# Performance work log

Hardware: AMD Instinct MI355X
Metric: run time of the kernel (lower is better)

Reference implementation:

```python
import jax, jax.numpy as jnp
import numpy as np

DIM = 256
HEADS = 8
SR = 2
EPS = 1e-5


def setup_inputs() -> dict:
    key = jax.random.key(0)
    ks = jax.random.split(key, 8)
    B, N, C = 4, 4096, DIM
    s = 0.02
    return {
        "x": jax.random.normal(ks[0], (B, N, C), dtype=jnp.float32),
        "H": 64,
        "W": 64,
        # sequence-reduction conv (Conv2d dim->dim, k=SR, stride=SR), OIHW
        "sr_w": jax.random.normal(ks[1], (C, C, SR, SR), dtype=jnp.float32) * s,
        "sr_b": jnp.zeros((C,), dtype=jnp.float32),
        "ln_g": jnp.ones((C,), dtype=jnp.float32),
        "ln_b": jnp.zeros((C,), dtype=jnp.float32),
        # torch Linear weights: y = x @ W.T (qkv_bias=False)
        "q_w": jax.random.normal(ks[2], (C, C), dtype=jnp.float32) * s,
        "kv_w": jax.random.normal(ks[3], (2 * C, C), dtype=jnp.float32) * s,
        "proj_w": jax.random.normal(ks[4], (C, C), dtype=jnp.float32) * s,
        "proj_b": jnp.zeros((C,), dtype=jnp.float32),
    }


def reference(x, H, W, sr_w, sr_b, ln_g, ln_b, q_w, kv_w, proj_w, proj_b):
    B, N, C = x.shape
    h, d = HEADS, C // HEADS
    scale = d ** -0.5

    # q: [B, h, N, d]
    q = (x @ q_w.T).reshape(B, N, h, d).transpose(0, 2, 1, 3)

    # sequence reduction: [B,N,C] -> [B,C,H,W] -> conv(k=SR, s=SR) -> [B, N', C]
    x_ = x.transpose(0, 2, 1).reshape(B, C, H, W)
    x_ = jax.lax.conv_general_dilated(
        x_, sr_w, window_strides=(SR, SR), padding="VALID",
        dimension_numbers=("NCHW", "OIHW", "NCHW"))
    x_ = x_ + sr_b[None, :, None, None]
    x_ = x_.reshape(B, C, -1).transpose(0, 2, 1)  # [B, N', C]

    # LayerNorm over C
    mu = x_.mean(-1, keepdims=True)
    var = x_.var(-1, keepdims=True)
    x_ = (x_ - mu) * jax.lax.rsqrt(var + EPS) * ln_g + ln_b

    # kv: [2, B, h, N', d]
    kv = (x_ @ kv_w.T).reshape(B, -1, 2, h, d).transpose(2, 0, 3, 1, 4)
    k, v = kv[0], kv[1]

    attn = jnp.einsum("bhnd,bhmd->bhnm", q, k) * scale
    attn = jax.nn.softmax(attn, axis=-1)  # attn_drop = 0 -> identity
    out = jnp.einsum("bhnm,bhmd->bhnd", attn, v)
    out = out.transpose(0, 2, 1, 3).reshape(B, N, C)

    return out @ proj_w.T + proj_b  # proj_drop = 0 -> identity
```

## Files before the change

### kernel.cpp

```cpp
#include <hip/hip_runtime.h>
#include <hip/hip_bf16.h>


typedef __attribute__((ext_vector_type(8))) short bf16x8;
typedef __attribute__((ext_vector_type(8))) unsigned short u16x8;
typedef __attribute__((ext_vector_type(4))) float f32x4;
typedef __attribute__((ext_vector_type(16))) float f32x16;
typedef __attribute__((ext_vector_type(2))) unsigned u32x2v;
typedef __attribute__((ext_vector_type(4))) unsigned u32x4v;

__device__ inline unsigned short f2bf(float f) {
  unsigned u = __float_as_uint(f);
  u += 0x7fffu + ((u >> 16) & 1u);
  return (unsigned short)(u >> 16);
}

__global__ __launch_bounds__(256) void prep_kernel(
    const float* __restrict__ srw, unsigned short* __restrict__ srw_bf) {
  const int o = blockIdx.x, t = threadIdx.x;
  float4 v = reinterpret_cast<const float4*>(srw + (size_t)o * 1024)[t];
  srw_bf[(size_t)o * 1024 + 0 * 256 + t] = f2bf(v.x);
  srw_bf[(size_t)o * 1024 + 1 * 256 + t] = f2bf(v.y);
  srw_bf[(size_t)o * 1024 + 2 * 256 + t] = f2bf(v.z);
  srw_bf[(size_t)o * 1024 + 3 * 256 + t] = f2bf(v.w);
}

__device__ __forceinline__ void gemm_body_q(
    const float* __restrict__ Af, const float* __restrict__ W,
    unsigned short* __restrict__ C, int K, int N, float oscale,
    int m0, int n0, unsigned short* Asb, unsigned short* Bsb) {
  const int tid = threadIdx.x;
  const int w = tid >> 6, l = tid & 63, c = l & 15, g = l >> 4;
  const int wr = w >> 1, wc = w & 1;
  const int ar = tid >> 1, ah = tid & 1;
  const int bn = tid >> 2, bq = tid & 3;

  f32x4 acc[4][2];
#pragma unroll
  for (int mt = 0; mt < 4; ++mt)
#pragma unroll
    for (int nt = 0; nt < 2; ++nt)
#pragma unroll
      for (int r = 0; r < 4; ++r) acc[mt][nt][r] = 0.f;

  for (int k0 = 0; k0 < K; k0 += 32) {
    __syncthreads();
    {
      const float* asrc = Af + (size_t)(m0 + ar) * K + k0 + ah * 16;
      float4 a0 = *reinterpret_cast<const float4*>(asrc);
      float4 a1 = *reinterpret_cast<const float4*>(asrc + 4);
      float4 a2 = *reinterpret_cast<const float4*>(asrc + 8);
      float4 a3 = *reinterpret_cast<const float4*>(asrc + 12);
      u16x8 w0, w1;
      w0[0] = f2bf(a0.x); w0[1] = f2bf(a0.y); w0[2] = f2bf(a0.z); w0[3] = f2bf(a0.w);
      w0[4] = f2bf(a1.x); w0[5] = f2bf(a1.y); w0[6] = f2bf(a1.z); w0[7] = f2bf(a1.w);
      w1[0] = f2bf(a2.x); w1[1] = f2bf(a2.y); w1[2] = f2bf(a2.z); w1[3] = f2bf(a2.w);
      w1[4] = f2bf(a3.x); w1[5] = f2bf(a3.y); w1[6] = f2bf(a3.z); w1[7] = f2bf(a3.w);
      *reinterpret_cast<u16x8*>(&Asb[ar * 40 + ah * 16]) = w0;
      *reinterpret_cast<u16x8*>(&Asb[ar * 40 + ah * 16 + 8]) = w1;
    }
    {
      const float* wsrc = W + (size_t)(n0 + bn) * K + k0 + bq * 8;
      float4 w0 = *reinterpret_cast<const float4*>(wsrc);
      float4 w1 = *reinterpret_cast<const float4*>(wsrc + 4);
      u16x8 wb;
      wb[0] = f2bf(w0.x); wb[1] = f2bf(w0.y); wb[2] = f2bf(w0.z); wb[3] = f2bf(w0.w);
      wb[4] = f2bf(w1.x); wb[5] = f2bf(w1.y); wb[6] = f2bf(w1.z); wb[7] = f2bf(w1.w);
      *reinterpret_cast<u16x8*>(&Bsb[bn * 40 + bq * 8]) = wb;
    }
    __syncthreads();
    bf16x8 af[4], bfr[2];
#pragma unroll
    for (int mt = 0; mt < 4; ++mt)
      af[mt] = *reinterpret_cast<const bf16x8*>(
          &Asb[(wr * 64 + mt * 16 + c) * 40 + g * 8]);
#pragma unroll
    for (int nt = 0; nt < 2; ++nt)
      bfr[nt] = *reinterpret_cast<const bf16x8*>(
          &Bsb[(wc * 32 + nt * 16 + c) * 40 + g * 8]);
#pragma unroll
    for (int mt = 0; mt < 4; ++mt)
#pragma unroll
      for (int nt = 0; nt < 2; ++nt)
        acc[mt][nt] = __builtin_amdgcn_mfma_f32_16x16x32_bf16(
            af[mt], bfr[nt], acc[mt][nt], 0, 0, 0);
  }

#pragma unroll
  for (int mt = 0; mt < 4; ++mt)
#pragma unroll
    for (int nt = 0; nt < 2; ++nt) {
      int row = m0 + wr * 64 + mt * 16 + g * 4;
      int col = n0 + wc * 32 + nt * 16 + c;
#pragma unroll
      for (int r = 0; r < 4; ++r)
        C[(size_t)(row + r) * N + col] = f2bf(acc[mt][nt][r] * oscale);
    }
}

__device__ __forceinline__ void conv_body(
    const float* __restrict__ Xf, const unsigned short* __restrict__ Wp,
    const float* __restrict__ bias, float* __restrict__ C,
    int m0, int n0, unsigned short* Asb, unsigned short* Bsb) {
  const int tid = threadIdx.x;
  const int w = tid >> 6, l = tid & 63, c = l & 15, g = l >> 4;
  const int wr = w >> 1, wc = w & 1;
  const int sr = tid >> 2, sh = tid & 3;

  int base[4];
  {
    int row = m0 + sr;
    int b = row >> 10, o = row & 1023, oh = o >> 5, ow = o & 31;
#pragma unroll
    for (int tap = 0; tap < 4; ++tap) {
      int n = ((oh << 1) + (tap >> 1)) * 64 + (ow << 1) + (tap & 1);
      base[tap] = ((b << 12) + n) << 8;
    }
  }

  f32x4 acc[2][2];
#pragma unroll
  for (int mt = 0; mt < 2; ++mt)
#pragma unroll
    for (int nt = 0; nt < 2; ++nt)
#pragma unroll
      for (int r = 0; r < 4; ++r) acc[mt][nt][r] = 0.f;

  for (int k0 = 0; k0 < 1024; k0 += 32) {
    const int tap = k0 >> 8, ci0 = (k0 & 255) + sh * 8;
    __syncthreads();
    {
      const float* xp = Xf + base[tap] + ci0;
      float4 a0 = *reinterpret_cast<const float4*>(xp);
      float4 a1 = *reinterpret_cast<const float4*>(xp + 4);
      u16x8 av;
      av[0] = f2bf(a0.x); av[1] = f2bf(a0.y); av[2] = f2bf(a0.z); av[3] = f2bf(a0.w);
      av[4] = f2bf(a1.x); av[5] = f2bf(a1.y); av[6] = f2bf(a1.z); av[7] = f2bf(a1.w);
      *reinterpret_cast<u16x8*>(&Asb[sr * 40 + sh * 8]) = av;
    }
    u16x8 wv = *reinterpret_cast<const u16x8*>(
        &Wp[(size_t)(n0 + sr) * 1024 + k0 + sh * 8]);
    *reinterpret_cast<u16x8*>(&Bsb[sr * 40 + sh * 8]) = wv;
    __syncthreads();
    bf16x8 af[2], bfr[2];
#pragma unroll
    for (int mt = 0; mt < 2; ++mt)
      af[mt] = *reinterpret_cast<const bf16x8*>(
          &Asb[(wr * 32 + mt * 16 + c) * 40 + g * 8]);
#pragma unroll
    for (int nt = 0; nt < 2; ++nt)
      bfr[nt] = *reinterpret_cast<const bf16x8*>(
          &Bsb[(wc * 32 + nt * 16 + c) * 40 + g * 8]);
#pragma unroll
    for (int mt = 0; mt < 2; ++mt)
#pragma unroll
      for (int nt = 0; nt < 2; ++nt)
        acc[mt][nt] = __builtin_amdgcn_mfma_f32_16x16x32_bf16(
            af[mt], bfr[nt], acc[mt][nt], 0, 0, 0);
  }

#pragma unroll
  for (int mt = 0; mt < 2; ++mt)
#pragma unroll
    for (int nt = 0; nt < 2; ++nt) {
      int row = m0 + wr * 32 + mt * 16 + g * 4;
      int col = n0 + wc * 32 + nt * 16 + c;
      float bv = bias[col];
#pragma unroll
      for (int r = 0; r < 4; ++r)
        C[(size_t)(row + r) * 256 + col] = acc[mt][nt][r] + bv;
    }
}

__global__ __launch_bounds__(256) void qconv_kernel(
    const float* __restrict__ x, const float* __restrict__ q_w,
    unsigned short* __restrict__ q_bf, const unsigned short* __restrict__ srw_bf,
    const float* __restrict__ sr_b, float* __restrict__ xred, float qscale) {
  __shared__ unsigned short smem[128 * 40 + 64 * 40];
  const int bid = blockIdx.x;
  if (bid < 512) {
    gemm_body_q(x, q_w, q_bf, 256, 256, qscale,
                (bid >> 2) * 128, (bid & 3) * 64, smem, smem + 128 * 40);
  } else {
    int cb = bid - 512;
    conv_body(x, srw_bf, sr_b, xred,
              (cb >> 2) * 64, (cb & 3) * 64, smem, smem + 64 * 40);
  }
}

__global__ __launch_bounds__(256) void kv_gemm(
    const unsigned short* __restrict__ A, const float* __restrict__ W,
    unsigned short* __restrict__ Kb, unsigned short* __restrict__ Vtp) {
  __shared__ unsigned short Asb[128 * 40];
  __shared__ unsigned short Bsb[64 * 40];
  const int tid = threadIdx.x;
  const int w = tid >> 6, l = tid & 63, c = l & 15, g = l >> 4;
  const int wr = w >> 1, wc = w & 1;
  const int m0 = blockIdx.y * 128, n0 = blockIdx.x * 64;
  const int ar = tid >> 1, ah = tid & 1;
  const int bn = tid >> 2, bq = tid & 3;
  const int K = 256;

  f32x4 acc[4][2];
#pragma unroll
  for (int mt = 0; mt < 4; ++mt)
#pragma unroll
    for (int nt = 0; nt < 2; ++nt)
#pragma unroll
      for (int r = 0; r < 4; ++r) acc[mt][nt][r] = 0.f;

  for (int k0 = 0; k0 < K; k0 += 32) {
    __syncthreads();
    {
      const unsigned short* asrc = A + (size_t)(m0 + ar) * K + k0 + ah * 16;
      u16x8 a0 = *reinterpret_cast<const u16x8*>(asrc);
      u16x8 a1 = *reinterpret_cast<const u16x8*>(asrc + 8);
      *reinterpret_cast<u16x8*>(&Asb[ar * 40 + ah * 16]) = a0;
      *reinterpret_cast<u16x8*>(&Asb[ar * 40 + ah * 16 + 8]) = a1;
    }
    {
      const float* wsrc = W + (size_t)(n0 + bn) * K + k0 + bq * 8;
      float4 w0 = *reinterpret_cast<const float4*>(wsrc);
      float4 w1 = *reinterpret_cast<const float4*>(wsrc + 4);
      u16x8 wb;
      wb[0] = f2bf(w0.x); wb[1] = f2bf(w0.y); wb[2] = f2bf(w0.z); wb[3] = f2bf(w0.w);
      wb[4] = f2bf(w1.x); wb[5] = f2bf(w1.y); wb[6] = f2bf(w1.z); wb[7] = f2bf(w1.w);
      *reinterpret_cast<u16x8*>(&Bsb[bn * 40 + bq * 8]) = wb;
    }
    __syncthreads();
    bf16x8 af[4], bfr[2];
#pragma unroll
    for (int mt = 0; mt < 4; ++mt)
      af[mt] = *reinterpret_cast<const bf16x8*>(
          &Asb[(wr * 64 + mt * 16 + c) * 40 + g * 8]);
#pragma unroll
    for (int nt = 0; nt < 2; ++nt)
      bfr[nt] = *reinterpret_cast<const bf16x8*>(
          &Bsb[(wc * 32 + nt * 16 + c) * 40 + g * 8]);
#pragma unroll
    for (int mt = 0; mt < 4; ++mt)
#pragma unroll
      for (int nt = 0; nt < 2; ++nt)
        acc[mt][nt] = __builtin_amdgcn_mfma_f32_16x16x32_bf16(
            af[mt], bfr[nt], acc[mt][nt], 0, 0, 0);
  }

#pragma unroll
  for (int mt = 0; mt < 4; ++mt)
#pragma unroll
    for (int nt = 0; nt < 2; ++nt) {
      int row = m0 + wr * 64 + mt * 16 + g * 4;
      int col = n0 + wc * 32 + nt * 16 + c;
#pragma unroll
      for (int r = 0; r < 4; ++r) {
        float v = acc[mt][nt][r];
        if (col < 256) {
          Kb[(size_t)(row + r) * 256 + col] = f2bf(v);
        } else {
          int head = (col - 256) >> 5, d = (col - 256) & 31;
          int rr = row + r;
          Vtp[((size_t)(((rr >> 10) << 3) + head) * 32 + d) * 1024 +
              (rr & 1023)] = f2bf(v);
        }
      }
    }
}

__global__ __launch_bounds__(256) void proj_gemm(
    const unsigned short* __restrict__ A, const float* __restrict__ W,
    const float* __restrict__ bias, float* __restrict__ C) {
  __shared__ unsigned short Asb[64 * 40];
  __shared__ unsigned short Bsb[64 * 40];
  const int tid = threadIdx.x;
  const int w = tid >> 6, l = tid & 63, c = l & 15, g = l >> 4;
  const int wr = w >> 1, wc = w & 1;
  const int m0 = blockIdx.y * 64, n0 = blockIdx.x * 64;
  const int sr = tid >> 2, sh = tid & 3;

  f32x4 acc[2][2];
#pragma unroll
  for (int mt = 0; mt < 2; ++mt)
#pragma unroll
    for (int nt = 0; nt < 2; ++nt)
#pragma unroll
      for (int r = 0; r < 4; ++r) acc[mt][nt][r] = 0.f;

  for (int k0 = 0; k0 < 256; k0 += 32) {
    __syncthreads();
    {
      u16x8 av = *reinterpret_cast<const u16x8*>(
          &A[(size_t)(m0 + sr) * 256 + k0 + sh * 8]);
      *reinterpret_cast<u16x8*>(&Asb[sr * 40 + sh * 8]) = av;
    }
    {
      const float* wsrc = W + (size_t)(n0 + sr) * 256 + k0 + sh * 8;
      float4 w0 = *reinterpret_cast<const float4*>(wsrc);
      float4 w1 = *reinterpret_cast<const float4*>(wsrc + 4);
      u16x8 wb;
      wb[0] = f2bf(w0.x); wb[1] = f2bf(w0.y); wb[2] = f2bf(w0.z); wb[3] = f2bf(w0.w);
      wb[4] = f2bf(w1.x); wb[5] = f2bf(w1.y); wb[6] = f2bf(w1.z); wb[7] = f2bf(w1.w);
      *reinterpret_cast<u16x8*>(&Bsb[sr * 40 + sh * 8]) = wb;
    }
    __syncthreads();
    bf16x8 af[2], bfr[2];
#pragma unroll
    for (int mt = 0; mt < 2; ++mt)
      af[mt] = *reinterpret_cast<const bf16x8*>(
          &Asb[(wr * 32 + mt * 16 + c) * 40 + g * 8]);
#pragma unroll
    for (int nt = 0; nt < 2; ++nt)
      bfr[nt] = *reinterpret_cast<const bf16x8*>(
          &Bsb[(wc * 32 + nt * 16 + c) * 40 + g * 8]);
#pragma unroll
    for (int mt = 0; mt < 2; ++mt)
#pragma unroll
      for (int nt = 0; nt < 2; ++nt)
        acc[mt][nt] = __builtin_amdgcn_mfma_f32_16x16x32_bf16(
            af[mt], bfr[nt], acc[mt][nt], 0, 0, 0);
  }

#pragma unroll
  for (int mt = 0; mt < 2; ++mt)
#pragma unroll
    for (int nt = 0; nt < 2; ++nt) {
      int row = m0 + wr * 32 + mt * 16 + g * 4;
      int col = n0 + wc * 32 + nt * 16 + c;
      float bv = bias[col];
#pragma unroll
      for (int r = 0; r < 4; ++r)
        C[(size_t)(row + r) * 256 + col] = acc[mt][nt][r] + bv;
    }
}

__global__ __launch_bounds__(256) void ln_kernel(
    const float* __restrict__ xr, const float* __restrict__ gam,
    const float* __restrict__ bet, unsigned short* __restrict__ xo) {
  const int w = threadIdx.x >> 6, l = threadIdx.x & 63;
  const int row = blockIdx.x * 4 + w;
  float4 v = *reinterpret_cast<const float4*>(xr + (size_t)row * 256 + l * 4);
  float s = (v.x + v.y) + (v.z + v.w);
  float s2 = (v.x * v.x + v.y * v.y) + (v.z * v.z + v.w * v.w);
#pragma unroll
  for (int off = 32; off > 0; off >>= 1) {
    s  += __shfl_xor(s, off, 64);
    s2 += __shfl_xor(s2, off, 64);
  }
  float mean = s * (1.f / 256.f);
  float var = s2 * (1.f / 256.f) - mean * mean;
  float rstd = rsqrtf(var + 1e-5f);
  float4 g = *reinterpret_cast<const float4*>(gam + l * 4);
  float4 bb = *reinterpret_cast<const float4*>(bet + l * 4);
  unsigned short o0 = f2bf((v.x - mean) * rstd * g.x + bb.x);
  unsigned short o1 = f2bf((v.y - mean) * rstd * g.y + bb.y);
  unsigned short o2 = f2bf((v.z - mean) * rstd * g.z + bb.z);
  unsigned short o3 = f2bf((v.w - mean) * rstd * g.w + bb.w);
  unsigned long long pk =
      (unsigned long long)o0 | ((unsigned long long)o1 << 16) |
      ((unsigned long long)o2 << 32) | ((unsigned long long)o3 << 48);
  *reinterpret_cast<unsigned long long*>(xo + (size_t)row * 256 + l * 4) = pk;
}

__global__ __launch_bounds__(256) void attn_mfma(
    const unsigned short* __restrict__ Qb,
    const unsigned short* __restrict__ Kb,
    const unsigned short* __restrict__ Vtg,
    unsigned short* __restrict__ O) {
  __shared__ __align__(16) unsigned short Kt[2][64][36];
  __shared__ __align__(16) unsigned short Vt[2][32][72];

  const int tid = threadIdx.x;
  const int l = tid & 63;
  const int w = tid >> 6;
  const int q32 = l & 31, hi = l >> 5;
  const int wg = blockIdx.x;
  const int qb = wg & 31, head = (wg >> 5) & 7, b = wg >> 8;
  const int hcol = head << 5;
  const int q0 = (b << 12) + (qb << 7) + (w << 5);

  bf16x8 qf[2];
  {
    const unsigned short* qp = Qb + (size_t)(q0 + q32) * 256 + hcol + hi * 8;
    qf[0] = *reinterpret_cast<const bf16x8*>(qp);
    qf[1] = *reinterpret_cast<const bf16x8*>(qp + 16);
  }

  const int sd = tid >> 3, skv = (tid & 7) << 3;
  const unsigned short* vtrow =
      Vtg + ((size_t)((b << 3) + head) * 32 + sd) * 1024 + skv;
  const int kr = tid >> 2, kh = (tid & 3) << 3;
  const unsigned short* ktrow =
      Kb + ((size_t)(b << 10) + kr) * 256 + hcol + kh;

  {
    u16x8 va = *reinterpret_cast<const u16x8*>(vtrow);
    *reinterpret_cast<u16x8*>(&Vt[0][sd][skv]) = va;
    u16x8 ka = *reinterpret_cast<const u16x8*>(ktrow);
    *reinterpret_cast<u16x8*>(&Kt[0][kr][kh]) = ka;
  }

  f32x16 acc;
#pragma unroll
  for (int r = 0; r < 16; ++r) acc[r] = 0.f;
  float lsum = 0.f;

  for (int t = 0; t < 16; ++t) {
    const int cur = t & 1;
    __syncthreads();

    u16x8 nv0, nk0;
    if (t < 15) {
      nv0 = *reinterpret_cast<const u16x8*>(vtrow + (t + 1) * 64);
      nk0 = *reinterpret_cast<const u16x8*>(ktrow + (size_t)(t + 1) * 64 * 256);
    }

    f32x16 s[2];
    {
      bf16x8 k00 = *reinterpret_cast<const bf16x8*>(&Kt[cur][q32][hi * 8]);
      bf16x8 k01 = *reinterpret_cast<const bf16x8*>(&Kt[cur][q32][hi * 8 + 16]);
      bf16x8 k10 = *reinterpret_cast<const bf16x8*>(&Kt[cur][q32 + 32][hi * 8]);
      bf16x8 k11 = *reinterpret_cast<const bf16x8*>(&Kt[cur][q32 + 32][hi * 8 + 16]);
      f32x16 z;
#pragma unroll
      for (int r = 0; r < 16; ++r) z[r] = 0.f;
      s[0] = __builtin_amdgcn_mfma_f32_32x32x16_bf16(k00, qf[0], z, 0, 0, 0);
      s[0] = __builtin_amdgcn_mfma_f32_32x32x16_bf16(k01, qf[1], s[0], 0, 0, 0);
      s[1] = __builtin_amdgcn_mfma_f32_32x32x16_bf16(k10, qf[0], z, 0, 0, 0);
      s[1] = __builtin_amdgcn_mfma_f32_32x32x16_bf16(k11, qf[1], s[1], 0, 0, 0);
    }

#pragma unroll
    for (int kvb = 0; kvb < 2; ++kvb) {
      float p16[16];
#pragma unroll
      for (int r = 0; r < 16; ++r)
        p16[r] = __builtin_amdgcn_exp2f(s[kvb][r]);
      float s0 = (p16[0] + p16[1]) + (p16[2] + p16[3]);
      float s1 = (p16[4] + p16[5]) + (p16[6] + p16[7]);
      float s2 = (p16[8] + p16[9]) + (p16[10] + p16[11]);
      float s3 = (p16[12] + p16[13]) + (p16[14] + p16[15]);
      lsum += (s0 + s1) + (s2 + s3);
      unsigned A[8];
#pragma unroll
      for (int i = 0; i < 8; ++i) {
        unsigned o;
        asm("v_cvt_pk_bf16_f32 %0, %1, %2"
            : "=v"(o) : "v"(p16[2 * i]), "v"(p16[2 * i + 1]));
        A[i] = o;
      }
      u32x2v r02 = __builtin_amdgcn_permlane32_swap(A[0], A[2], false, false);
      u32x2v r13 = __builtin_amdgcn_permlane32_swap(A[1], A[3], false, false);
      u32x2v r46 = __builtin_amdgcn_permlane32_swap(A[4], A[6], false, false);
      u32x2v r57 = __builtin_amdgcn_permlane32_swap(A[5], A[7], false, false);
      u32x4v pk0 = {r02[0], r13[0], r02[1], r13[1]};
      u32x4v pk1 = {r46[0], r57[0], r46[1], r57[1]};
      bf16x8 pf0 = __builtin_bit_cast(bf16x8, pk0);
      bf16x8 pf1 = __builtin_bit_cast(bf16x8, pk1);
      const unsigned short* vrow = &Vt[cur][q32][kvb * 32 + hi * 8];
      bf16x8 vf0 = *reinterpret_cast<const bf16x8*>(vrow);
      bf16x8 vf1 = *reinterpret_cast<const bf16x8*>(vrow + 16);
      acc = __builtin_amdgcn_mfma_f32_32x32x16_bf16(vf0, pf0, acc, 0, 0, 0);
      acc = __builtin_amdgcn_mfma_f32_32x32x16_bf16(vf1, pf1, acc, 0, 0, 0);
    }

    if (t < 15) {
      *reinterpret_cast<u16x8*>(&Vt[cur ^ 1][sd][skv]) = nv0;
      *reinterpret_cast<u16x8*>(&Kt[cur ^ 1][kr][kh]) = nk0;
    }
  }

  lsum += __shfl_xor(lsum, 32, 64);
  float inv = 1.f / lsum;
  unsigned short* orow = O + (size_t)(q0 + q32) * 256 + hcol;
#pragma unroll
  for (int rb = 0; rb < 4; ++rb) {
    const int d0 = rb * 8 + hi * 4;
    float a0 = acc[rb * 4 + 0] * inv, a1 = acc[rb * 4 + 1] * inv;
    float a2 = acc[rb * 4 + 2] * inv, a3 = acc[rb * 4 + 3] * inv;
    unsigned w0, w1;
    asm("v_cvt_pk_bf16_f32 %0, %1, %2" : "=v"(w0) : "v"(a0), "v"(a1));
    asm("v_cvt_pk_bf16_f32 %0, %1, %2" : "=v"(w1) : "v"(a2), "v"(a3));
    unsigned long long pk = (unsigned long long)w0 | ((unsigned long long)w1 << 32);
    *reinterpret_cast<unsigned long long*>(orow + d0) = pk;
  }
}

extern "C" void kernel_launch(void* const* d_in, const int* in_sizes, int n_in,
                              void* d_out, int out_size, void* d_ws,
                              size_t ws_size, hipStream_t stream) {
  const float* x      = (const float*)d_in[0];
  const float* sr_w   = (const float*)d_in[3];
  const float* sr_b   = (const float*)d_in[4];
  const float* ln_g   = (const float*)d_in[5];
  const float* ln_b   = (const float*)d_in[6];
  const float* q_w    = (const float*)d_in[7];
  const float* kv_w   = (const float*)d_in[8];
  const float* proj_w = (const float*)d_in[9];
  const float* proj_b = (const float*)d_in[10];
  float* out = (float*)d_out;

  char* ws = (char*)d_ws;
  unsigned short* q_bf    = (unsigned short*)(ws);
  unsigned short* srw_bf  = (unsigned short*)(ws + 8388608);
  float*          xred    = (float*)(ws + 8912896);
  unsigned short* x_ln    = (unsigned short*)(ws + 13107200);
  unsigned short* k_buf   = (unsigned short*)(ws + 15204352);
  unsigned short* vt_buf  = (unsigned short*)(ws + 17301504);
  unsigned short* attn_bf = (unsigned short*)(ws + 19398656);

  const float qscale = 0.25506975154985854f;

  prep_kernel<<<256, 256, 0, stream>>>(sr_w, srw_bf);
  qconv_kernel<<<768, 256, 0, stream>>>(
      x, q_w, q_bf, srw_bf, sr_b, xred, qscale);
  ln_kernel<<<1024, 256, 0, stream>>>(xred, ln_g, ln_b, x_ln);
  kv_gemm<<<dim3(8, 32), 256, 0, stream>>>(x_ln, kv_w, k_buf, vt_buf);
  attn_mfma<<<1024, 256, 0, stream>>>(q_bf, k_buf, vt_buf, attn_bf);
  proj_gemm<<<dim3(4, 256), 256, 0, stream>>>(attn_bf, proj_w, proj_b, out);
}
```

Measured before the change: 92.34 us.

## Double-buffer LDS tiles with register prefetch in all GEMM and conv loops

Converts the q GEMM, conv, kv GEMM and proj GEMM main loops to double-buffered shared-memory tiles. The next K-slice is loaded from global memory into registers before the MFMAs on the current slice, then written into the alternate buffer afterwards. This leaves one barrier per iteration instead of two and hides global load latency behind the math. In exchange it doubles LDS use and raises register pressure, which may lower occupancy.

After: 88.79 us. 3.8% less time.

```diff
diff --git a/kernel.cpp b/kernel.cpp
--- a/kernel.cpp
+++ b/kernel.cpp
@@ -13,6 +13,13 @@
   unsigned u = __float_as_uint(f);
   u += 0x7fffu + ((u >> 16) & 1u);
   return (unsigned short)(u >> 16);
+}
+
+__device__ inline u16x8 cast8(float4 a, float4 b) {
+  u16x8 r;
+  r[0] = f2bf(a.x); r[1] = f2bf(a.y); r[2] = f2bf(a.z); r[3] = f2bf(a.w);
+  r[4] = f2bf(b.x); r[5] = f2bf(b.y); r[6] = f2bf(b.z); r[7] = f2bf(b.w);
+  return r;
 }
 
 __global__ __launch_bounds__(256) void prep_kernel(
@@ -27,13 +34,18 @@
 
 __device__ __forceinline__ void gemm_body_q(
     const float* __restrict__ Af, const float* __restrict__ W,
-    unsigned short* __restrict__ C, int K, int N, float oscale,
+    unsigned short* __restrict__ C, float oscale,
     int m0, int n0, unsigned short* Asb, unsigned short* Bsb) {
+  const int K = 256, N = 256, NK = 8;
   const int tid = threadIdx.x;
   const int w = tid >> 6, l = tid & 63, c = l & 15, g = l >> 4;
   const int wr = w >> 1, wc = w & 1;
   const int ar = tid >> 1, ah = tid & 1;
   const int bn = tid >> 2, bq = tid & 3;
+  const int ABUF = 128 * 40, BBUF = 64 * 40;
+
+  const float* aptr = Af + (size_t)(m0 + ar) * K + ah * 16;
+  const float* wptr = W + (size_t)(n0 + bn) * K + bq * 8;
 
   f32x4 acc[4][2];
 #pragma unroll
@@ -43,47 +55,53 @@
 #pragma unroll
       for (int r = 0; r < 4; ++r) acc[mt][nt][r] = 0.f;
 
-  for (int k0 = 0; k0 < K; k0 += 32) {
+  {
+    float4 a0 = *reinterpret_cast<const float4*>(aptr);
+    float4 a1 = *reinterpret_cast<const float4*>(aptr + 4);
+    float4 a2 = *reinterpret_cast<const float4*>(aptr + 8);
+    float4 a3 = *reinterpret_cast<const float4*>(aptr + 12);
+    float4 w0 = *reinterpret_cast<const float4*>(wptr);
+    float4 w1 = *reinterpret_cast<const float4*>(wptr + 4);
+    *reinterpret_cast<u16x8*>(&Asb[ar * 40 + ah * 16]) = cast8(a0, a1);
+    *reinterpret_cast<u16x8*>(&Asb[ar * 40 + ah * 16 + 8]) = cast8(a2, a3);
+    *reinterpret_cast<u16x8*>(&Bsb[bn * 40 + bq * 8]) = cast8(w0, w1);
+  }
+
+  for (int t = 0; t < NK; ++t) {
+    const int cur = t & 1;
     __syncthreads();
-    {
-      const float* asrc = Af + (size_t)(m0 + ar) * K + k0 + ah * 16;
-      float4 a0 = *reinterpret_cast<const float4*>(asrc);
-      float4 a1 = *reinterpret_cast<const float4*>(asrc + 4);
-      float4 a2 = *reinterpret_cast<const float4*>(asrc + 8);
-      float4 a3 = *reinterpret_cast<const float4*>(asrc + 12);
-      u16x8 w0, w1;
-      w0[0] = f2bf(a0.x); w0[1] = f2bf(a0.y); w0[2] = f2bf(a0.z); w0[3] = f2bf(a0.w);
-      w0[4] = f2bf(a1.x); w0[5] = f2bf(a1.y); w0[6] = f2bf(a1.z); w0[7] = f2bf(a1.w);
-      w1[0] = f2bf(a2.x); w1[1] = f2bf(a2.y); w1[2] = f2bf(a2.z); w1[3] = f2bf(a2.w);
-      w1[4] = f2bf(a3.x); w1[5] = f2bf(a3.y); w1[6] = f2bf(a3.z); w1[7] = f2bf(a3.w);
-      *reinterpret_cast<u16x8*>(&Asb[ar * 40 + ah * 16]) = w0;
-      *reinterpret_cast<u16x8*>(&Asb[ar * 40 + ah * 16 + 8]) = w1;
-    }
-    {
-      const float* wsrc = W + (size_t)(n0 + bn) * K + k0 + bq * 8;
-      float4 w0 = *reinterpret_cast<const float4*>(wsrc);
-      float4 w1 = *reinterpret_cast<const float4*>(wsrc + 4);
-      u16x8 wb;
-      wb[0] = f2bf(w0.x); wb[1] = f2bf(w0.y); wb[2] = f2bf(w0.z); wb[3] = f2bf(w0.w);
-      wb[4] = f2bf(w1.x); wb[5] = f2bf(w1.y); wb[6] = f2bf(w1.z); wb[7] = f2bf(w1.w);
-      *reinterpret_cast<u16x8*>(&Bsb[bn * 40 + bq * 8]) = wb;
-    }
-    __syncthreads();
+    float4 na0, na1, na2, na3, nw0, nw1;
+    if (t < NK - 1) {
+      const float* ap = aptr + (t + 1) * 32;
+      na0 = *reinterpret_cast<const float4*>(ap);
+      na1 = *reinterpret_cast<const float4*>(ap + 4);
+      na2 = *reinterpret_cast<const float4*>(ap + 8);
+      na3 = *reinterpret_cast<const float4*>(ap + 12);
+      const float* wp = wptr + (t + 1) * 32;
+      nw0 = *reinterpret_cast<const float4*>(wp);
+      nw1 = *reinterpret_cast<const float4*>(wp + 4);
+    }
     bf16x8 af[4], bfr[2];
 #pragma unroll
     for (int mt = 0; mt < 4; ++mt)
       af[mt] = *reinterpret_cast<const bf16x8*>(
-          &Asb[(wr * 64 + mt * 16 + c) * 40 + g * 8]);
+          &Asb[cur * ABUF + (wr * 64 + mt * 16 + c) * 40 + g * 8]);
 #pragma unroll
     for (int nt = 0; nt < 2; ++nt)
       bfr[nt] = *reinterpret_cast<const bf16x8*>(
-          &Bsb[(wc * 32 + nt * 16 + c) * 40 + g * 8]);
+          &Bsb[cur * BBUF + (wc * 32 + nt * 16 + c) * 40 + g * 8]);
 #pragma unroll
     for (int mt = 0; mt < 4; ++mt)
 #pragma unroll
       for (int nt = 0; nt < 2; ++nt)
         acc[mt][nt] = __builtin_amdgcn_mfma_f32_16x16x32_bf16(
             af[mt], bfr[nt], acc[mt][nt], 0, 0, 0);
+    if (t < NK - 1) {
+      const int nxt = cur ^ 1;
+      *reinterpret_cast<u16x8*>(&Asb[nxt * ABUF + ar * 40 + ah * 16]) = cast8(na0, na1);
+      *reinterpret_cast<u16x8*>(&Asb[nxt * ABUF + ar * 40 + ah * 16 + 8]) = cast8(na2, na3);
+      *reinterpret_cast<u16x8*>(&Bsb[nxt * BBUF + bn * 40 + bq * 8]) = cast8(nw0, nw1);
+    }
   }
 
 #pragma unroll
@@ -102,10 +120,12 @@
     const float* __restrict__ Xf, const unsigned short* __restrict__ Wp,
     const float* __restrict__ bias, float* __restrict__ C,
     int m0, int n0, unsigned short* Asb, unsigned short* Bsb) {
+  const int NK = 32;
   const int tid = threadIdx.x;
   const int w = tid >> 6, l = tid & 63, c = l & 15, g = l >> 4;
   const int wr = w >> 1, wc = w & 1;
   const int sr = tid >> 2, sh = tid & 3;
+  const int BUF = 64 * 40;
 
   int base[4];
   {
@@ -117,6 +137,7 @@
       base[tap] = ((b << 12) + n) << 8;
     }
   }
+  const unsigned short* wptr = Wp + (size_t)(n0 + sr) * 1024 + sh * 8;
 
   f32x4 acc[2][2];
 #pragma unroll
@@ -126,37 +147,46 @@
 #pragma unroll
       for (int r = 0; r < 4; ++r) acc[mt][nt][r] = 0.f;
 
-  for (int k0 = 0; k0 < 1024; k0 += 32) {
-    const int tap = k0 >> 8, ci0 = (k0 & 255) + sh * 8;
+  {
+    const float* xp = Xf + base[0] + sh * 8;
+    float4 a0 = *reinterpret_cast<const float4*>(xp);
+    float4 a1 = *reinterpret_cast<const float4*>(xp + 4);
+    *reinterpret_cast<u16x8*>(&Asb[sr * 40 + sh * 8]) = cast8(a0, a1);
+    *reinterpret_cast<u16x8*>(&Bsb[sr * 40 + sh * 8]) =
+        *reinterpret_cast<const u16x8*>(wptr);
+  }
+
+  for (int t = 0; t < NK; ++t) {
+    const int cur = t & 1;
     __syncthreads();
-    {
-      const float* xp = Xf + base[tap] + ci0;
-      float4 a0 = *reinterpret_cast<const float4*>(xp);
-      float4 a1 = *reinterpret_cast<const float4*>(xp + 4);
-      u16x8 av;
-      av[0] = f2bf(a0.x); av[1] = f2bf(a0.y); av[2] = f2bf(a0.z); av[3] = f2bf(a0.w);
-      av[4] = f2bf(a1.x); av[5] = f2bf(a1.y); av[6] = f2bf(a1.z); av[7] = f2bf(a1.w);
-      *reinterpret_cast<u16x8*>(&Asb[sr * 40 + sh * 8]) = av;
-    }
-    u16x8 wv = *reinterpret_cast<const u16x8*>(
-        &Wp[(size_t)(n0 + sr) * 1024 + k0 + sh * 8]);
-    *reinterpret_cast<u16x8*>(&Bsb[sr * 40 + sh * 8]) = wv;
-    __syncthreads();
+    float4 na0, na1; u16x8 nw;
+    if (t < NK - 1) {
+      const int k0n = (t + 1) * 32;
+      const float* xp = Xf + base[k0n >> 8] + (k0n & 255) + sh * 8;
+      na0 = *reinterpret_cast<const float4*>(xp);
+      na1 = *reinterpret_cast<const float4*>(xp + 4);
+      nw = *reinterpret_cast<const u16x8*>(wptr + (t + 1) * 32);
+    }
     bf16x8 af[2], bfr[2];
 #pragma unroll
     for (int mt = 0; mt < 2; ++mt)
       af[mt] = *reinterpret_cast<const bf16x8*>(
-          &Asb[(wr * 32 + mt * 16 + c) * 40 + g * 8]);
+          &Asb[cur * BUF + (wr * 32 + mt * 16 + c) * 40 + g * 8]);
 #pragma unroll
     for (int nt = 0; nt < 2; ++nt)
       bfr[nt] = *reinterpret_cast<const bf16x8*>(
-          &Bsb[(wc * 32 + nt * 16 + c) * 40 + g * 8]);
+          &Bsb[cur * BUF + (wc * 32 + nt * 16 + c) * 40 + g * 8]);
 #pragma unroll
     for (int mt = 0; mt < 2; ++mt)
 #pragma unroll
       for (int nt = 0; nt < 2; ++nt)
         acc[mt][nt] = __builtin_amdgcn_mfma_f32_16x16x32_bf16(
             af[mt], bfr[nt], acc[mt][nt], 0, 0, 0);
+    if (t < NK - 1) {
+      const int nxt = cur ^ 1;
+      *reinterpret_cast<u16x8*>(&Asb[nxt * BUF + sr * 40 + sh * 8]) = cast8(na0, na1);
+      *reinterpret_cast<u16x8*>(&Bsb[nxt * BUF + sr * 40 + sh * 8]) = nw;
+    }
   }
 
 #pragma unroll
@@ -176,30 +206,34 @@
     const float* __restrict__ x, const float* __restrict__ q_w,
     unsigned short* __restrict__ q_bf, const unsigned short* __restrict__ srw_bf,
     const float* __restrict__ sr_b, float* __restrict__ xred, float qscale) {
-  __shared__ unsigned short smem[128 * 40 + 64 * 40];
+  __shared__ unsigned short smem[2 * 128 * 40 + 2 * 64 * 40];
   const int bid = blockIdx.x;
   if (bid < 512) {
-    gemm_body_q(x, q_w, q_bf, 256, 256, qscale,
-                (bid >> 2) * 128, (bid & 3) * 64, smem, smem + 128 * 40);
+    gemm_body_q(x, q_w, q_bf, qscale,
+                (bid >> 2) * 128, (bid & 3) * 64, smem, smem + 2 * 128 * 40);
   } else {
     int cb = bid - 512;
     conv_body(x, srw_bf, sr_b, xred,
-              (cb >> 2) * 64, (cb & 3) * 64, smem, smem + 64 * 40);
+              (cb >> 2) * 64, (cb & 3) * 64, smem, smem + 2 * 64 * 40);
   }
 }
 
 __global__ __launch_bounds__(256) void kv_gemm(
     const unsigned short* __restrict__ A, const float* __restrict__ W,
     unsigned short* __restrict__ Kb, unsigned short* __restrict__ Vtp) {
-  __shared__ unsigned short Asb[128 * 40];
-  __shared__ unsigned short Bsb[64 * 40];
+  __shared__ unsigned short Asb[2 * 128 * 40];
+  __shared__ unsigned short Bsb[2 * 64 * 40];
+  const int K = 256, NK = 8;
   const int tid = threadIdx.x;
   const int w = tid >> 6, l = tid & 63, c = l & 15, g = l >> 4;
   const int wr = w >> 1, wc = w & 1;
   const int m0 = blockIdx.y * 128, n0 = blockIdx.x * 64;
   const int ar = tid >> 1, ah = tid & 1;
   const int bn = tid >> 2, bq = tid & 3;
-  const int K = 256;
+  const int ABUF = 128 * 40, BBUF = 64 * 40;
+
+  const unsigned short* aptr = A + (size_t)(m0 + ar) * K + ah * 16;
+  const float* wptr = W + (size_t)(n0 + bn) * K + bq * 8;
 
   f32x4 acc[4][2];
 #pragma unroll
@@ -209,40 +243,49 @@
 #pragma unroll
       for (int r = 0; r < 4; ++r) acc[mt][nt][r] = 0.f;
 
-  for (int k0 = 0; k0 < K; k0 += 32) {
+  {
+    u16x8 a0 = *reinterpret_cast<const u16x8*>(aptr);
+    u16x8 a1 = *reinterpret_cast<const u16x8*>(aptr + 8);
+    float4 w0 = *reinterpret_cast<const float4*>(wptr);
+    float4 w1 = *reinterpret_cast<const float4*>(wptr + 4);
+    *reinterpret_cast<u16x8*>(&Asb[ar * 40 + ah * 16]) = a0;
+    *reinterpret_cast<u16x8*>(&Asb[ar * 40 + ah * 16 + 8]) = a1;
+    *reinterpret_cast<u16x8*>(&Bsb[bn * 40 + bq * 8]) = cast8(w0, w1);
+  }
+
+  for (int t = 0; t < NK; ++t) {
+    const int cur = t & 1;
     __syncthreads();
-    {
-      const unsigned short* asrc = A + (size_t)(m0 + ar) * K + k0 + ah * 16;
-      u16x8 a0 = *reinterpret_cast<const u16x8*>(asrc);
-      u16x8 a1 = *reinterpret_cast<const u16x8*>(asrc + 8);
-      *reinterpret_cast<u16x8*>(&Asb[ar * 40 + ah * 16]) = a0;
-      *reinterpret_cast<u16x8*>(&Asb[ar * 40 + ah * 16 + 8]) = a1;
-    }
-    {
-      const float* wsrc = W + (size_t)(n0 + bn) * K + k0 + bq * 8;
-      float4 w0 = *reinterpret_cast<const float4*>(wsrc);
-      float4 w1 = *reinterpret_cast<const float4*>(wsrc + 4);
-      u16x8 wb;
-      wb[0] = f2bf(w0.x); wb[1] = f2bf(w0.y); wb[2] = f2bf(w0.z); wb[3] = f2bf(w0.w);
-      wb[4] = f2bf(w1.x); wb[5] = f2bf(w1.y); wb[6] = f2bf(w1.z); wb[7] = f2bf(w1.w);
-      *reinterpret_cast<u16x8*>(&Bsb[bn * 40 + bq * 8]) = wb;
-    }
-    __syncthreads();
+    u16x8 na0, na1; float4 nw0, nw1;
+    if (t < NK - 1) {
+      const unsigned short* ap = aptr + (t + 1) * 32;
+      na0 = *reinterpret_cast<const u16x8*>(ap);
+      na1 = *reinterpret_cast<const u16x8*>(ap + 8);
+      const float* wp = wptr + (t + 1) * 32;
+      nw0 = *reinterpret_cast<const float4*>(wp);
+      nw1 = *reinterpret_cast<const float4*>(wp + 4);
+    }
     bf16x8 af[4], bfr[2];
 #pragma unroll
     for (int mt = 0; mt < 4; ++mt)
       af[mt] = *reinterpret_cast<const bf16x8*>(
-          &Asb[(wr * 64 + mt * 16 + c) * 40 + g * 8]);
+          &Asb[cur * ABUF + (wr * 64 + mt * 16 + c) * 40 + g * 8]);
 #pragma unroll
     for (int nt = 0; nt < 2; ++nt)
       bfr[nt] = *reinterpret_cast<const bf16x8*>(
-          &Bsb[(wc * 32 + nt * 16 + c) * 40 + g * 8]);
+          &Bsb[cur * BBUF + (wc * 32 + nt * 16 + c) * 40 + g * 8]);
 #pragma unroll
     for (int mt = 0; mt < 4; ++mt)
 #pragma unroll
       for (int nt = 0; nt < 2; ++nt)
         acc[mt][nt] = __builtin_amdgcn_mfma_f32_16x16x32_bf16(
             af[mt], bfr[nt], acc[mt][nt], 0, 0, 0);
+    if (t < NK - 1) {
+      const int nxt = cur ^ 1;
+      *reinterpret_cast<u16x8*>(&Asb[nxt * ABUF + ar * 40 + ah * 16]) = na0;
+      *reinterpret_cast<u16x8*>(&Asb[nxt * ABUF + ar * 40 + ah * 16 + 8]) = na1;
+      *reinterpret_cast<u16x8*>(&Bsb[nxt * BBUF + bn * 40 + bq * 8]) = cast8(nw0, nw1);
+    }
   }
 
 #pragma unroll
@@ -269,13 +312,18 @@
 __global__ __launch_bounds__(256) void proj_gemm(
     const unsigned short* __restrict__ A, const float* __restrict__ W,
     const float* __restrict__ bias, float* __restrict__ C) {
-  __shared__ unsigned short Asb[64 * 40];
-  __shared__ unsigned short Bsb[64 * 40];
+  __shared__ unsigned short Asb[2 * 64 * 40];
+  __shared__ unsigned short Bsb[2 * 64 * 40];
+  const int NK = 8;
   const int tid = threadIdx.x;
   const int w = tid >> 6, l = tid & 63, c = l & 15, g = l >> 4;
   const int wr = w >> 1, wc = w & 1;
   const int m0 = blockIdx.y * 64, n0 = blockIdx.x * 64;
   const int sr = tid >> 2, sh = tid & 3;
+  const int BUF = 64 * 40;
+
+  const unsigned short* aptr = A + (size_t)(m0 + sr) * 256 + sh * 8;
+  const float* wptr = W + (size_t)(n0 + sr) * 256 + sh * 8;
 
   f32x4 acc[2][2];
 #pragma unroll
@@ -285,38 +333,44 @@
 #pragma unroll
       for (int r = 0; r < 4; ++r) acc[mt][nt][r] = 0.f;
 
-  for (int k0 = 0; k0 < 256; k0 += 32) {
+  {
+    u16x8 av = *reinterpret_cast<const u16x8*>(aptr);
+    float4 w0 = *reinterpret_cast<const float4*>(wptr);
+    float4 w1 = *reinterpret_cast<const float4*>(wptr + 4);
+    *reinterpret_cast<u16x8*>(&Asb[sr * 40 + sh * 8]) = av;
+    *reinterpret_cast<u16x8*>(&Bsb[sr * 40 + sh * 8]) = cast8(w0, w1);
+  }
+
+  for (int t = 0; t < NK; ++t) {
+    const int cur = t & 1;
     __syncthreads();
-    {
-      u16x8 av = *reinterpret_cast<const u16x8*>(
-          &A[(size_t)(m0 + sr) * 256 + k0 + sh * 8]);
-      *reinterpret_cast<u16x8*>(&Asb[sr * 40 + sh * 8]) = av;
-    }
-    {
-      const float* wsrc = W + (size_t)(n0 + sr) * 256 + k0 + sh * 8;
-      float4 w0 = *reinterpret_cast<const float4*>(wsrc);
-      float4 w1 = *reinterpret_cast<const float4*>(wsrc + 4);
-      u16x8 wb;
-      wb[0] = f2bf(w0.x); wb[1] = f2bf(w0.y); wb[2] = f2bf(w0.z); wb[3] = f2bf(w0.w);
-      wb[4] = f2bf(w1.x); wb[5] = f2bf(w1.y); wb[6] = f2bf(w1.z); wb[7] = f2bf(w1.w);
-      *reinterpret_cast<u16x8*>(&Bsb[sr * 40 + sh * 8]) = wb;
-    }
-    __syncthreads();
+    u16x8 na; float4 nw0, nw1;
+    if (t < NK - 1) {
+      na = *reinterpret_cast<const u16x8*>(aptr + (t + 1) * 32);
+      const float* wp = wptr + (t + 1) * 32;
+      nw0 = *reinterpret_cast<const float4*>(wp);
+      nw1 = *reinterpret_cast<const float4*>(wp + 4);
+    }
     bf16x8 af[2], bfr[2];
 #pragma unroll
     for (int mt = 0; mt < 2; ++mt)
       af[mt] = *reinterpret_cast<const bf16x8*>(
-          &Asb[(wr * 32 + mt * 16 + c) * 40 + g * 8]);
+          &Asb[cur * BUF + (wr * 32 + mt * 16 + c) * 40 + g * 8]);
 #pragma unroll
     for (int nt = 0; nt < 2; ++nt)
       bfr[nt] = *reinterpret_cast<const bf16x8*>(
-          &Bsb[(wc * 32 + nt * 16 + c) * 40 + g * 8]);
+          &Bsb[cur * BUF + (wc * 32 + nt * 16 + c) * 40 + g * 8]);
 #pragma unroll
     for (int mt = 0; mt < 2; ++mt)
 #pragma unroll
       for (int nt = 0; nt < 2; ++nt)
         acc[mt][nt] = __builtin_amdgcn_mfma_f32_16x16x32_bf16(
             af[mt], bfr[nt], acc[mt][nt], 0, 0, 0);
+    if (t < NK - 1) {
+      const int nxt = cur ^ 1;
+      *reinterpret_cast<u16x8*>(&Asb[nxt * BUF + sr * 40 + sh * 8]) = na;
+      *reinterpret_cast<u16x8*>(&Bsb[nxt * BUF + sr * 40 + sh * 8]) = cast8(nw0, nw1);
+    }
   }
 
 #pragma unroll
```
